# Performance work log

Measured on AMD Instinct MI355X. Metric: run time of the kernel, lower is better.

Reference implementation:

```python
import jax, jax.numpy as jnp
import numpy as np

RADIUS = 0.4
NSHELLS = 3
GSCALE = 0.69314718056 * NSHELLS ** 2  # ln(2)*num_shells^2, as in TFN.__init__
KNN = 32          # patch_size
UNITS = 64        # per-type intertwiner width
STRIDE = 4        # source->target pooling ratio (num_points[i]/num_points[i+1])


def real_sh(d):
    """Real spherical harmonics up to l=3 on unit vectors d[...,3] -> [...,16]."""
    x, y, z = d[..., 0], d[..., 1], d[..., 2]
    x2, y2, z2 = x * x, y * y, z * z
    comps = [
        0.282095 * jnp.ones_like(x),                 # l=0
        0.488603 * y, 0.488603 * z, 0.488603 * x,    # l=1 (y,z,x)
        1.092548 * x * y,                            # l=2
        1.092548 * y * z,
        0.315392 * (3.0 * z2 - 1.0),
        1.092548 * x * z,
        0.546274 * (x2 - y2),
        0.590044 * y * (3.0 * x2 - y2),              # l=3
        2.890611 * x * y * z,
        0.457046 * y * (5.0 * z2 - 1.0),
        0.373176 * z * (5.0 * z2 - 3.0),
        0.457046 * x * (5.0 * z2 - 1.0),
        1.445306 * z * (x2 - y2),
        0.590044 * x * (x2 - 3.0 * y2),
    ]
    return jnp.stack(comps, axis=-1)


def setup_inputs() -> dict:
    key = jax.random.key(0)
    ks = jax.random.split(key, 16)
    B, N, C = 32, 2048, 64
    SC = NSHELLS * C  # channels after shell expansion
    FEAT = 4 * UNITS  # invariant feature dim (types 0..3)
    NUM_CLASSES = 40
    inp = {
        "points": jax.random.normal(ks[0], (B, N, 3), jnp.float32),
        "feats": 0.1 * jax.random.normal(ks[1], (B, N, C), jnp.float32),
        "W0": jax.random.normal(ks[2], (SC, UNITS), jnp.float32) / np.sqrt(SC),
        "b0": jnp.zeros((UNITS,), jnp.float32),
        "W1": jax.random.normal(ks[3], (SC, UNITS), jnp.float32) / np.sqrt(SC),
        "W2": jax.random.normal(ks[4], (SC, UNITS), jnp.float32) / np.sqrt(SC),
        "W3": jax.random.normal(ks[5], (SC, UNITS), jnp.float32) / np.sqrt(SC),
        "Wfc1": jax.random.normal(ks[6], (FEAT, 512), jnp.float32) / np.sqrt(FEAT),
        "bfc1": jnp.zeros((512,), jnp.float32),
        "Wfc2": jax.random.normal(ks[7], (512, 256), jnp.float32) / np.sqrt(512),
        "bfc2": jnp.zeros((256,), jnp.float32),
        "Wsm": jax.random.normal(ks[8], (256, NUM_CLASSES), jnp.float32) / np.sqrt(256),
        "bsm": jnp.zeros((NUM_CLASSES,), jnp.float32),
    }
    return inp


def reference(points, feats, W0, b0, W1, W2, W3, Wfc1, bfc1, Wfc2, bfc2, Wsm, bsm):
    # --- pooling: strided subsample (kd_pooling analogue) ---
    target = points[:, ::STRIDE]                       # [B,M,3]
    # --- ball-query style grouping: knn gather ---
    d2 = jnp.sum((target[:, :, None, :] - points[:, None, :, :]) ** 2, axis=-1)  # [B,M,N]
    _, idx = jax.lax.top_k(-d2, KNN)                   # [B,M,K]
    gat = jax.vmap(lambda a, i: a[i])
    p = gat(points, idx)                               # [B,M,K,3]
    f = gat(feats, idx)                                # [B,M,K,C]
    rel = p - target[:, :, None, :]
    dist = jnp.sqrt(jnp.maximum(jnp.sum(rel * rel, axis=-1), 1e-12))  # [B,M,K]
    dirs = rel / dist[..., None]
    # --- spherical-harmonic Gaussian shell kernels ---
    Y = real_sh(dirs)                                  # [B,M,K,16]
    centers = jnp.linspace(0.0, 1.0, NSHELLS)
    dn = dist / RADIUS
    w = jnp.exp(-GSCALE * (dn[..., None] - centers) ** 2)
    w = w * (dn <= 1.0)[..., None]                     # bounded kernel
    w = w / (jnp.sum(w, axis=2, keepdims=True) + 1e-8)  # normalize over patch
    kern = w[..., :, None] * Y[..., None, :]           # [B,M,K,S,16]
    # --- point conv: contract over patch dim ---
    z = jnp.einsum('bmksp,bmkc->bmpsc', kern, f)       # [B,M,16,S,C]
    B_, M_ = z.shape[:2]
    z = z.reshape(B_, M_, 16, -1)                      # [B,M,16,S*C]
    # --- per-type Dense intertwiners (bias only on type-0) + invariant norms ---
    slabs = [(0, 1, W0, b0), (1, 4, W1, None), (4, 9, W2, None), (9, 16, W3, None)]
    outs = []
    for s, e, W, b in slabs:
        o = z[:, :, s:e, :] @ W
        if b is not None:
            o = o + b
        outs.append(jnp.sqrt(jnp.maximum(jnp.sum(o * o, axis=2), 1e-8)))  # [B,M,U]
    h = jnp.concatenate(outs, axis=-1)                 # [B,M,4U]
    h = jnp.max(h, axis=1)                             # global max pool
    # --- MLP head ---
    h = jax.nn.relu(h @ Wfc1 + bfc1)
    h = jax.nn.relu(h @ Wfc2 + bfc2)
    return jax.nn.softmax(h @ Wsm + bsm, axis=-1)
```

## Files before the change

### kernel.cpp

```cpp
#include <hip/hip_runtime.h>
#include <hip/hip_bf16.h>
#include <math.h>

#define B_ 32
#define N_ 2048
#define C_ 64
#define M_ 512
#define KNN_ 32
#define RADIUS_ 0.4f
#define RCUT2 0.16016f
#define GSCALE_ 6.2383246250f
#define TT 4
#define SEGCAP 40
#define NBLK 4096

typedef __attribute__((ext_vector_type(8))) short bf16x8;
typedef __attribute__((ext_vector_type(4))) float f32x4;
union FragU { uint4 q; bf16x8 h; unsigned int u[4]; };

#define CAND_OFF 0
#define CNT_OFF  1280
#define ZT_ 3144
#define RST 196
#define FSH 560
#define FSL 1616
#define WGT_OFF  12576
#define WGT_TS   96
#define SM_TOTAL 12960

__device__ inline void split2(float a, unsigned& hi, unsigned& lo) {
    unsigned ab = __float_as_uint(a);
    float res = a - __uint_as_float(ab & 0xffff0000u);
    __hip_bfloat16 lb = __float2bfloat16(res);
    hi = ab >> 16;
    lo = *(unsigned short*)&lb;
}

__device__ inline unsigned cvt_pk_bf16(float a, float b) {
    unsigned r;
    asm("v_cvt_pk_bf16_f32 %0, %1, %2" : "=v"(r) : "v"(a), "v"(b));
    return r;
}

__device__ inline void split_pair(float a0, float a1, unsigned& hw, unsigned& lw) {
    hw = cvt_pk_bf16(a0, a1);
    float r0 = a0 - __uint_as_float(hw << 16);
    float r1 = a1 - __uint_as_float(hw & 0xffff0000u);
    lw = cvt_pk_bf16(r0, r1);
}

__device__ inline unsigned pack_hl(float a) {
    unsigned t = cvt_pk_bf16(a, a);
    unsigned hfu = t << 16;
    float res = a - __uint_as_float(hfu);
    return cvt_pk_bf16(__uint_as_float(hfu), res);
}

__global__ __launch_bounds__(256) void wsplit_kernel(
    const float* __restrict__ W0, const float* __restrict__ W1,
    const float* __restrict__ W2, const float* __restrict__ W3,
    uint4* __restrict__ Wb)
{
    int gid = blockIdx.x * 256 + threadIdx.x;
    int lane = gid & 63, frag = gid >> 6;
    int v = frag & 1, nt = (frag >> 1) & 3;
    int ls = frag >> 3, ks = ls % 6, l = ls / 6;
    const float* W = (l==0) ? W0 : (l==1) ? W1 : (l==2) ? W2 : W3;
    int n = nt*16 + (lane & 15), quad = lane >> 4;
    unsigned int d[4];
    #pragma unroll
    for (int dd = 0; dd < 4; ++dd) {
        unsigned int two[2];
        #pragma unroll
        for (int e = 0; e < 2; ++e) {
            int k = ks*32 + quad*8 + dd*2 + e;
            unsigned hi, lo;
            split2(W[k*64 + n], hi, lo);
            two[e] = (v == 0) ? hi : lo;
        }
        d[dd] = two[0] | (two[1] << 16);
    }
    Wb[(size_t)frag*64 + lane] = make_uint4(d[0], d[1], d[2], d[3]);
}

__global__ __launch_bounds__(256, 3) void main_kernel(
    const float* __restrict__ points, const float* __restrict__ feats,
    const float* __restrict__ b0, const uint4* __restrict__ Wb,
    unsigned int* __restrict__ hmax,
    const float* __restrict__ Wfc1, const float* __restrict__ Wfc2,
    float* __restrict__ dummy)
{
    __shared__ __align__(16) float smem[SM_TOTAL];
    __shared__ int sh_nbr[TT][32];
    __shared__ int sh_cnt[TT];
    unsigned int* smemU = (unsigned int*)smem;
    const int tid = threadIdx.x;
    const int b = blockIdx.x >> 7;
    const int mbase = (blockIdx.x & 127) * TT;
    const float* pb = points + (size_t)b * N_ * 3;
    const int wv = tid >> 6, lane = tid & 63;

    float wm1 = Wfc1[(size_t)blockIdx.x*32 + (tid & 31)];
    float wm2 = Wfc2[(size_t)blockIdx.x*32 + (tid & 31)];

    float b0r[4];
    #pragma unroll
    for (int nt = 0; nt < 4; ++nt) b0r[nt] = b0[nt*16 + (lane & 15)];

    {
        unsigned long long* cand = (unsigned long long*)&smem[CAND_OFF];
        int* cntk = (int*)&smem[CNT_OFF];
        float tx[TT], ty[TT], tz[TT];
        #pragma unroll
        for (int c = 0; c < TT; ++c) {
            int m4 = 4*(mbase + c);
            tx[c] = pb[3*m4]; ty[c] = pb[3*m4+1]; tz[c] = pb[3*m4+2];
        }
        float px[8], py[8], pz[8];
        const float* ps = pb + 3*(wv*512 + lane);
        #pragma unroll
        for (int it = 0; it < 8; ++it) {
            px[it] = ps[it*192+0]; py[it] = ps[it*192+1]; pz[it] = ps[it*192+2];
        }
        int bcnt[TT];
        #pragma unroll
        for (int c = 0; c < TT; ++c) bcnt[c] = 0;
        #pragma unroll
        for (int it = 0; it < 8; ++it) {
            int i = wv*512 + it*64 + lane;
            #pragma unroll
            for (int c = 0; c < TT; ++c) {
                float dx = px[it] - tx[c], dy = py[it] - ty[c], dz = pz[it] - tz[c];
                float d2 = fmaf(dx,dx, fmaf(dy,dy, dz*dz));
                bool isc = d2 <= RCUT2;
                unsigned long long mk = __ballot(isc);
                if (isc) {
                    int pos = bcnt[c] + __popcll(mk & ((1ull<<lane)-1ull));
                    if (pos < SEGCAP)
                        cand[(size_t)(wv*TT+c)*SEGCAP + pos] =
                            ((unsigned long long)__float_as_uint(d2) << 32) | (unsigned)i;
                }
                bcnt[c] += __popcll(mk);
            }
        }
        if (lane == 0) {
            #pragma unroll
            for (int c = 0; c < TT; ++c)
                cntk[wv*TT+c] = bcnt[c] < SEGCAP ? bcnt[c] : SEGCAP;
        }
        __syncthreads();
        {
            const int t = wv;
            int c0 = cntk[0*TT+t], c1 = cntk[1*TT+t], c2 = cntk[2*TT+t], c3 = cntk[3*TT+t];
            int o1 = c0, o2 = c0+c1, o3 = c0+c1+c2;
            int C = o3 + c3; C = C < 128 ? C : 128;
            auto fetch = [&](int pos) -> unsigned long long {
                if (pos >= C) return ~0ull;
                int ws = (pos >= o1) + (pos >= o2) + (pos >= o3);
                int base = (ws==0) ? 0 : (ws==1) ? o1 : (ws==2) ? o2 : o3;
                return cand[(size_t)(ws*TT+t)*SEGCAP + (pos - base)];
            };
            unsigned long long kv0 = fetch(lane), kv1 = fetch(64 + lane);
            const unsigned long long lmask = (1ull << lane) - 1ull;
            if (C <= KNN_) {
                if (lane < KNN_) sh_nbr[t][lane] = (lane < C) ? (int)(kv0 & 0xffffffffu) : 0;
                if (lane == 0) sh_cnt[t] = C;
            } else {
                unsigned d0 = (unsigned)(kv0 >> 32);
                unsigned d1 = (unsigned)(kv1 >> 32);
                unsigned thr = 0u;
                for (int bit = 29; bit >= 0; --bit) {
                    unsigned mid = thr | (1u << bit);
                    int cnt = __popcll(__ballot(d0 < mid)) + __popcll(__ballot(d1 < mid));
                    if (cnt < KNN_) thr = mid;
                }
                bool le0 = d0 < thr, le1 = d1 < thr;
                int cntL = __popcll(__ballot(le0)) + __popcll(__ballot(le1));
                int E = KNN_ - cntL;
                unsigned long long me0 = __ballot(d0 == thr);
                unsigned long long me1 = __ballot(d1 == thr);
                int e0 = __popcll(me0);
                bool sel0 = le0 || ((d0 == thr) && (__popcll(me0 & lmask) < E));
                bool sel1 = le1 || ((d1 == thr) && (e0 + __popcll(me1 & lmask) < E));
                unsigned long long ms0 = __ballot(sel0);
                if (sel0) sh_nbr[t][__popcll(ms0 & lmask)] = (int)(kv0 & 0xffffffffu);
                int base0 = __popcll(ms0);
                unsigned long long ms1 = __ballot(sel1);
                if (sel1) sh_nbr[t][base0 + __popcll(ms1 & lmask)] = (int)(kv1 & 0xffffffffu);
                if (lane == 0) sh_cnt[t] = KNN_;
            }
        }
    }
    __syncthreads();

    if (tid < TT*32) {
        int t = tid >> 5, k = tid & 31;
        int n = sh_nbr[t][k];
        int m4 = 4*(mbase + t);
        float x = pb[3*n]   - pb[3*m4];
        float y = pb[3*n+1] - pb[3*m4+1];
        float z = pb[3*n+2] - pb[3*m4+2];
        float d2 = x*x + y*y + z*z;
        float dist = sqrtf(fmaxf(d2, 1e-12f));
        float inv = 1.0f / dist;
        float dx = x*inv, dy = y*inv, dz = z*inv;
        float x2 = dx*dx, y2 = dy*dy, z2 = dz*dz;
        float yv[16];
        yv[0]  = 0.282095f;
        yv[1]  = 0.488603f*dy;  yv[2] = 0.488603f*dz;  yv[3] = 0.488603f*dx;
        yv[4]  = 1.092548f*dx*dy;
        yv[5]  = 1.092548f*dy*dz;
        yv[6]  = 0.315392f*(3.0f*z2-1.0f);
        yv[7]  = 1.092548f*dx*dz;
        yv[8]  = 0.546274f*(x2-y2);
        yv[9]  = 0.590044f*dy*(3.0f*x2-y2);
        yv[10] = 2.890611f*dx*dy*dz;
        yv[11] = 0.457046f*dy*(5.0f*z2-1.0f);
        yv[12] = 0.373176f*dz*(5.0f*z2-3.0f);
        yv[13] = 0.457046f*dx*(5.0f*z2-1.0f);
        yv[14] = 1.445306f*dz*(x2-y2);
        yv[15] = 0.590044f*dx*(x2-3.0f*y2);
        float* Yp = &smem[t*ZT_ + k*17];
        #pragma unroll
        for (int p = 0; p < 16; ++p) Yp[p] = yv[p];
        float dn = dist * (1.0f/RADIUS_);
        bool ok = (k < sh_cnt[t]) && (dn <= 1.0f);
        float w0 = 0.f, w1 = 0.f, w2 = 0.f;
        if (ok) {
            float dd0 = dn, dd1 = dn - 0.5f, dd2 = dn - 1.0f;
            w0 = __expf(-GSCALE_*dd0*dd0);
            w1 = __expf(-GSCALE_*dd1*dd1);
            w2 = __expf(-GSCALE_*dd2*dd2);
        }
        float s0 = w0, s1 = w1, s2 = w2;
        #pragma unroll
        for (int off = 16; off >= 1; off >>= 1) {
            s0 += __shfl_xor(s0, off);
            s1 += __shfl_xor(s1, off);
            s2 += __shfl_xor(s2, off);
        }
        w0 /= (s0 + 1e-8f);
        w1 /= (s1 + 1e-8f);
        w2 /= (s2 + 1e-8f);
        smem[WGT_OFF + t*WGT_TS +      k] = w0;
        smem[WGT_OFF + t*WGT_TS + 32 + k] = w1;
        smem[WGT_OFF + t*WGT_TS + 64 + k] = w2;
    }
    {
        const float* fb = feats + (size_t)b * N_ * C_;
        const int t = wv;
        #pragma unroll
        for (int k2 = 0; k2 < 16; ++k2) {
            float f0 = fb[(size_t)sh_nbr[t][2*k2]   * C_ + lane];
            float f1 = fb[(size_t)sh_nbr[t][2*k2+1] * C_ + lane];
            unsigned hw, lw;
            split_pair(f0, f1, hw, lw);
            smemU[t*ZT_ + FSH + k2*66 + lane] = hw;
            smemU[t*ZT_ + FSL + k2*66 + lane] = lw;
        }
    }
    __syncthreads();

    {
        const int t = wv;
        const int quad = lane >> 4, col = lane & 15;
        float yv8[8];
        #pragma unroll
        for (int d = 0; d < 8; ++d)
            yv8[d] = smem[t*ZT_ + (quad*8 + d)*17 + col];
        FragU ah[3], al[3];
        #pragma unroll
        for (int s = 0; s < 3; ++s) {
            #pragma unroll
            for (int i = 0; i < 4; ++i) {
                float we = smem[WGT_OFF + t*WGT_TS + s*32 + quad*8 + 2*i];
                float wo = smem[WGT_OFF + t*WGT_TS + s*32 + quad*8 + 2*i + 1];
                split_pair(yv8[2*i]*we, yv8[2*i+1]*wo, ah[s].u[i], al[s].u[i]);
            }
        }
        f32x4 acc[3][4];
        #pragma unroll
        for (int s = 0; s < 3; ++s)
            #pragma unroll
            for (int nl = 0; nl < 4; ++nl) acc[s][nl] = (f32x4){0.f,0.f,0.f,0.f};
        #pragma unroll
        for (int nl = 0; nl < 4; ++nl) {
            int n = nl*16 + col;
            FragU bh, bl;
            #pragma unroll
            for (int i = 0; i < 4; ++i) {
                int k2 = quad*4 + i;
                bh.u[i] = smemU[t*ZT_ + FSH + k2*66 + n];
                bl.u[i] = smemU[t*ZT_ + FSL + k2*66 + n];
            }
            #pragma unroll
            for (int s = 0; s < 3; ++s) {
                acc[s][nl] = __builtin_amdgcn_mfma_f32_16x16x32_bf16(ah[s].h, bh.h, acc[s][nl], 0, 0, 0);
                acc[s][nl] = __builtin_amdgcn_mfma_f32_16x16x32_bf16(ah[s].h, bl.h, acc[s][nl], 0, 0, 0);
                acc[s][nl] = __builtin_amdgcn_mfma_f32_16x16x32_bf16(al[s].h, bh.h, acc[s][nl], 0, 0, 0);
            }
        }
        #pragma unroll
        for (int s = 0; s < 3; ++s) {
            #pragma unroll
            for (int nl = 0; nl < 4; ++nl) {
                #pragma unroll
                for (int r = 0; r < 4; ++r) {
                    int p = quad*4 + r;
                    smemU[t*ZT_ + p*RST + s*64 + nl*16 + col] = pack_hl(acc[s][nl][r]);
                }
            }
        }
    }
    __syncthreads();

    {
        const int bp0[4] = {0,1,4,9};
        const int bsz[4] = {1,3,5,7};
        const int band = wv;
        const int sz = bsz[band], p0 = bp0[band];
        const int rows = 2*sz;
        const int quad = lane >> 4, col = lane & 15;
        int gc = col < rows-1 ? col : rows-1;
        int tA = gc >= sz ? 1 : 0;
        int pA = p0 + gc - tA*sz;
        const unsigned baseA = tA*ZT_ + pA*RST;
        const unsigned baseB = baseA + 2*ZT_;
        f32x4 accA[4], accB[4];
        #pragma unroll
        for (int nt = 0; nt < 4; ++nt) {
            accA[nt] = (f32x4){0.f,0.f,0.f,0.f};
            accB[nt] = (f32x4){0.f,0.f,0.f,0.f};
        }

        #pragma unroll
        for (int ks = 0; ks < 6; ++ks) {
            const uint4* zpA = (const uint4*)&smemU[baseA + ks*32 + quad*8];
            const uint4* zpB = (const uint4*)&smemU[baseB + ks*32 + quad*8];
            uint4 a0q = zpA[0], a1q = zpA[1];
            uint4 c0q = zpB[0], c1q = zpB[1];
            FragU ahA, alA, ahB, alB;
            ahA.u[0] = __builtin_amdgcn_perm(a0q.y, a0q.x, 0x05040100u);
            ahA.u[1] = __builtin_amdgcn_perm(a0q.w, a0q.z, 0x05040100u);
            ahA.u[2] = __builtin_amdgcn_perm(a1q.y, a1q.x, 0x05040100u);
            ahA.u[3] = __builtin_amdgcn_perm(a1q.w, a1q.z, 0x05040100u);
            alA.u[0] = __builtin_amdgcn_perm(a0q.y, a0q.x, 0x07060302u);
            alA.u[1] = __builtin_amdgcn_perm(a0q.w, a0q.z, 0x07060302u);
            alA.u[2] = __builtin_amdgcn_perm(a1q.y, a1q.x, 0x07060302u);
            alA.u[3] = __builtin_amdgcn_perm(a1q.w, a1q.z, 0x07060302u);
            ahB.u[0] = __builtin_amdgcn_perm(c0q.y, c0q.x, 0x05040100u);
            ahB.u[1] = __builtin_amdgcn_perm(c0q.w, c0q.z, 0x05040100u);
            ahB.u[2] = __builtin_amdgcn_perm(c1q.y, c1q.x, 0x05040100u);
            ahB.u[3] = __builtin_amdgcn_perm(c1q.w, c1q.z, 0x05040100u);
            alB.u[0] = __builtin_amdgcn_perm(c0q.y, c0q.x, 0x07060302u);
            alB.u[1] = __builtin_amdgcn_perm(c0q.w, c0q.z, 0x07060302u);
            alB.u[2] = __builtin_amdgcn_perm(c1q.y, c1q.x, 0x07060302u);
            alB.u[3] = __builtin_amdgcn_perm(c1q.w, c1q.z, 0x07060302u);
            #pragma unroll
            for (int nt = 0; nt < 4; ++nt) {
                int fbase = ((band*6 + ks)*4 + nt)*2;
                FragU bh, bl;
                bh.q = Wb[(size_t)(fbase + 0)*64 + lane];
                bl.q = Wb[(size_t)(fbase + 1)*64 + lane];
                accA[nt] = __builtin_amdgcn_mfma_f32_16x16x32_bf16(ahA.h, bh.h, accA[nt], 0, 0, 0);
                accA[nt] = __builtin_amdgcn_mfma_f32_16x16x32_bf16(ahA.h, bl.h, accA[nt], 0, 0, 0);
                accA[nt] = __builtin_amdgcn_mfma_f32_16x16x32_bf16(alA.h, bh.h, accA[nt], 0, 0, 0);
                accB[nt] = __builtin_amdgcn_mfma_f32_16x16x32_bf16(ahB.h, bh.h, accB[nt], 0, 0, 0);
                accB[nt] = __builtin_amdgcn_mfma_f32_16x16x32_bf16(ahB.h, bl.h, accB[nt], 0, 0, 0);
                accB[nt] = __builtin_amdgcn_mfma_f32_16x16x32_bf16(alB.h, bh.h, accB[nt], 0, 0, 0);
            }
        }
        float sq[4][4];
        #pragma unroll
        for (int nt = 0; nt < 4; ++nt)
            #pragma unroll
            for (int tg = 0; tg < 4; ++tg) sq[nt][tg] = 0.f;
        #pragma unroll
        for (int r = 0; r < 4; ++r) {
            int row = quad*4 + r;
            bool valid = row < rows;
            int tt = row >= sz ? 1 : 0;
            #pragma unroll
            for (int nt = 0; nt < 4; ++nt) {
                float oA = accA[nt][r], oB = accB[nt][r];
                if (band == 0) { oA += b0r[nt]; oB += b0r[nt]; }
                if (valid) {
                    sq[nt][tt]   += oA*oA;
                    sq[nt][2+tt] += oB*oB;
                }
            }
        }
        #pragma unroll
        for (int nt = 0; nt < 4; ++nt) {
            #pragma unroll
            for (int tg = 0; tg < 4; ++tg) {
                float v = sq[nt][tg];
                v += __shfl_xor(v, 16);
                v += __shfl_xor(v, 32);
                sq[nt][tg] = v;
            }
        }
        if (quad == 0) {
            #pragma unroll
            for (int nt = 0; nt < 4; ++nt) {
                float h0 = sqrtf(fmaxf(sq[nt][0], 1e-8f));
                float h1 = sqrtf(fmaxf(sq[nt][1], 1e-8f));
                float h2 = sqrtf(fmaxf(sq[nt][2], 1e-8f));
                float h3 = sqrtf(fmaxf(sq[nt][3], 1e-8f));
                float mx = fmaxf(fmaxf(h0, h1), fmaxf(h2, h3));
                atomicMax(&hmax[b*256 + band*64 + nt*16 + col],
                          __float_as_uint(mx) ^ 0x80000000u);
            }
        }
    }

    if (__float_as_uint(wm1 + wm2) == 0xdeadbeefu) dummy[0] = wm1;
}

__global__ __launch_bounds__(256) void fc1_kernel(
    const unsigned int* __restrict__ hmaxk,
    const float* __restrict__ Wfc1, const float* __restrict__ bfc1,
    float* __restrict__ t1)
{
    __shared__ float h[256];
    __shared__ float red[4][80];
    const int b = blockIdx.x >> 3, uc = blockIdx.x & 7;
    const int tid = threadIdx.x;
    const int u = tid & 63, iq = tid >> 6;
    h[tid] = __uint_as_float(hmaxk[b*256 + tid] ^ 0x80000000u);
    __syncthreads();
    float acc = 0.f;
    const float* Wp = Wfc1 + uc*64 + u;
    #pragma unroll 8
    for (int i = iq*64; i < iq*64 + 64; ++i)
        acc = fmaf(h[i], Wp[(size_t)i*512], acc);
    red[iq][u] = acc;
    __syncthreads();
    if (iq == 0) {
        float s = red[0][u] + red[1][u] + red[2][u] + red[3][u] + bfc1[uc*64 + u];
        t1[b*512 + uc*64 + u] = fmaxf(s, 0.f);
    }
}

__global__ __launch_bounds__(256) void fc2_kernel(
    const float* __restrict__ t1,
    const float* __restrict__ Wfc2, const float* __restrict__ bfc2,
    float* __restrict__ t2)
{
    __shared__ float t1s[512];
    __shared__ float red[4][80];
    const int b = blockIdx.x >> 2, uc = blockIdx.x & 3;
    const int tid = threadIdx.x;
    const int u = tid & 63, isl = tid >> 6;
    t1s[tid]       = t1[b*512 + tid];
    t1s[256 + tid] = t1[b*512 + 256 + tid];
    __syncthreads();
    float acc = 0.f;
    const float* Wp = Wfc2 + uc*64 + u;
    #pragma unroll 8
    for (int i = isl*128; i < isl*128 + 128; ++i)
        acc = fmaf(t1s[i], Wp[(size_t)i*256], acc);
    red[isl][u] = acc;
    __syncthreads();
    if (isl == 0) {
        float s = red[0][u] + red[1][u] + red[2][u] + red[3][u] + bfc2[uc*64 + u];
        t2[b*256 + uc*64 + u] = fmaxf(s, 0.f);
    }
}

__global__ __launch_bounds__(256) void fc3_kernel(
    const float* __restrict__ t2,
    const float* __restrict__ Wsm, const float* __restrict__ bsm,
    float* __restrict__ out)
{
    __shared__ float t2s[256];
    __shared__ float red[4][80];
    const int b = blockIdx.x;
    const int tid = threadIdx.x;
    const int u = tid & 63, isl = tid >> 6;
    t2s[tid] = t2[b*256 + tid];
    __syncthreads();
    float acc = 0.f;
    if (u < 40) {
        #pragma unroll 8
        for (int i = isl*64; i < isl*64 + 64; ++i)
            acc = fmaf(t2s[i], Wsm[(size_t)i*40 + u], acc);
    }
    red[isl][u] = acc;
    __syncthreads();
    if (tid < 64) {
        float s = red[0][tid] + red[1][tid] + red[2][tid] + red[3][tid];
        float x = (tid < 40) ? (s + bsm[tid]) : -1e30f;
        float mx = x;
        #pragma unroll
        for (int off = 32; off >= 1; off >>= 1) mx = fmaxf(mx, __shfl_xor(mx, off));
        float e = (tid < 40) ? expf(x - mx) : 0.f;
        float ssum = e;
        #pragma unroll
        for (int off = 32; off >= 1; off >>= 1) ssum += __shfl_xor(ssum, off);
        if (tid < 40) out[b*40 + tid] = e / ssum;
    }
}

extern "C" void kernel_launch(void* const* d_in, const int* in_sizes, int n_in,
                              void* d_out, int out_size, void* d_ws, size_t ws_size,
                              hipStream_t stream)
{
    const float* points = (const float*)d_in[0];
    const float* feats  = (const float*)d_in[1];
    const float* W0   = (const float*)d_in[2];
    const float* b0   = (const float*)d_in[3];
    const float* W1   = (const float*)d_in[4];
    const float* W2   = (const float*)d_in[5];
    const float* W3   = (const float*)d_in[6];
    const float* Wfc1 = (const float*)d_in[7];
    const float* bfc1 = (const float*)d_in[8];
    const float* Wfc2 = (const float*)d_in[9];
    const float* bfc2 = (const float*)d_in[10];
    const float* Wsm  = (const float*)d_in[11];
    const float* bsm  = (const float*)d_in[12];
    float* out = (float*)d_out;

    char* ws = (char*)d_ws;
    unsigned int* hmax = (unsigned int*)ws;
    float* t1 = (float*)(ws + 32*1024);
    float* t2 = (float*)(ws + 96*1024);
    float* dummy = (float*)(ws + 120*1024);
    uint4* Wb = (uint4*)(ws + 128*1024);

    wsplit_kernel<<<48, 256, 0, stream>>>(W0, W1, W2, W3, Wb);
    main_kernel<<<NBLK, 256, 0, stream>>>(points, feats, b0, Wb, hmax,
                                          Wfc1, Wfc2, dummy);
    fc1_kernel<<<256, 256, 0, stream>>>(hmax, Wfc1, bfc1, t1);
    fc2_kernel<<<128, 256, 0, stream>>>(t1, Wfc2, bfc2, t2);
    fc3_kernel<<<32, 256, 0, stream>>>(t2, Wsm, bsm, out);
}
```

Measured before the change: 189.4 us.

## Process eight targets per 512-thread block and reuse weight fragments across targets

Doubles targets per block from four to eight, launching half as many blocks of 512 threads. In the MFMA stage each wave handles one band and half the output columns for all eight targets, so each loaded weight fragment feeds four target pairs instead of two. The per-target geometry and spherical-harmonic work is merged into the feature-gather phase, which removes one barrier and lets feature loads overlap with that math. The trade-off is more shared memory per block and lower block-level occupancy (two blocks per CU), plus a longer eight-segment candidate merge.

```diff
diff --git a/kernel.cpp b/kernel.cpp
--- a/kernel.cpp
+++ b/kernel.cpp
@@ -10,23 +10,22 @@
 #define RADIUS_ 0.4f
 #define RCUT2 0.16016f
 #define GSCALE_ 6.2383246250f
-#define TT 4
+#define TT 8
 #define SEGCAP 40
-#define NBLK 4096
+#define NBLK 2048
 
 typedef __attribute__((ext_vector_type(8))) short bf16x8;
 typedef __attribute__((ext_vector_type(4))) float f32x4;
 union FragU { uint4 q; bf16x8 h; unsigned int u[4]; };
 
-#define CAND_OFF 0
-#define CNT_OFF  1280
 #define ZT_ 3144
 #define RST 196
 #define FSH 560
 #define FSL 1616
-#define WGT_OFF  12576
+#define CAND_OFF 18864
+#define WGT_OFF  25152
 #define WGT_TS   96
-#define SM_TOTAL 12960
+#define SM_TOTAL 25920
 
 __device__ inline void split2(float a, unsigned& hi, unsigned& lo) {
     unsigned ab = __float_as_uint(a);
@@ -83,7 +82,7 @@
     Wb[(size_t)frag*64 + lane] = make_uint4(d[0], d[1], d[2], d[3]);
 }
 
-__global__ __launch_bounds__(256, 3) void main_kernel(
+__global__ __launch_bounds__(512, 2) void main_kernel(
     const float* __restrict__ points, const float* __restrict__ feats,
     const float* __restrict__ b0, const uint4* __restrict__ Wb,
     unsigned int* __restrict__ hmax,
@@ -93,41 +92,43 @@
     __shared__ __align__(16) float smem[SM_TOTAL];
     __shared__ int sh_nbr[TT][32];
     __shared__ int sh_cnt[TT];
+    __shared__ int cntk[64];
     unsigned int* smemU = (unsigned int*)smem;
     const int tid = threadIdx.x;
-    const int b = blockIdx.x >> 7;
-    const int mbase = (blockIdx.x & 127) * TT;
+    const int b = blockIdx.x >> 6;
+    const int mbase = (blockIdx.x & 63) * TT;
     const float* pb = points + (size_t)b * N_ * 3;
     const int wv = tid >> 6, lane = tid & 63;
 
-    float wm1 = Wfc1[(size_t)blockIdx.x*32 + (tid & 31)];
-    float wm2 = Wfc2[(size_t)blockIdx.x*32 + (tid & 31)];
-
-    float b0r[4];
+    float wm1 = Wfc1[(size_t)blockIdx.x*64 + (tid & 63)];
+    float wm2 = Wfc2[(size_t)blockIdx.x*64 + (tid & 63)];
+
+    const int nh_pre = wv >> 2;
+    float b0r[2];
     #pragma unroll
-    for (int nt = 0; nt < 4; ++nt) b0r[nt] = b0[nt*16 + (lane & 15)];
+    for (int ntl = 0; ntl < 2; ++ntl)
+        b0r[ntl] = b0[(nh_pre*2 + ntl)*16 + (lane & 15)];
 
     {
         unsigned long long* cand = (unsigned long long*)&smem[CAND_OFF];
-        int* cntk = (int*)&smem[CNT_OFF];
         float tx[TT], ty[TT], tz[TT];
         #pragma unroll
         for (int c = 0; c < TT; ++c) {
             int m4 = 4*(mbase + c);
             tx[c] = pb[3*m4]; ty[c] = pb[3*m4+1]; tz[c] = pb[3*m4+2];
         }
-        float px[8], py[8], pz[8];
-        const float* ps = pb + 3*(wv*512 + lane);
-        #pragma unroll
-        for (int it = 0; it < 8; ++it) {
+        float px[4], py[4], pz[4];
+        const float* ps = pb + 3*(wv*256 + lane);
+        #pragma unroll
+        for (int it = 0; it < 4; ++it) {
             px[it] = ps[it*192+0]; py[it] = ps[it*192+1]; pz[it] = ps[it*192+2];
         }
         int bcnt[TT];
         #pragma unroll
         for (int c = 0; c < TT; ++c) bcnt[c] = 0;
         #pragma unroll
-        for (int it = 0; it < 8; ++it) {
-            int i = wv*512 + it*64 + lane;
+        for (int it = 0; it < 4; ++it) {
+            int i = wv*256 + it*64 + lane;
             #pragma unroll
             for (int c = 0; c < TT; ++c) {
                 float dx = px[it] - tx[c], dy = py[it] - ty[c], dz = pz[it] - tz[c];
@@ -148,121 +149,130 @@
             for (int c = 0; c < TT; ++c)
                 cntk[wv*TT+c] = bcnt[c] < SEGCAP ? bcnt[c] : SEGCAP;
         }
-        __syncthreads();
-        {
-            const int t = wv;
-            int c0 = cntk[0*TT+t], c1 = cntk[1*TT+t], c2 = cntk[2*TT+t], c3 = cntk[3*TT+t];
-            int o1 = c0, o2 = c0+c1, o3 = c0+c1+c2;
-            int C = o3 + c3; C = C < 128 ? C : 128;
-            auto fetch = [&](int pos) -> unsigned long long {
-                if (pos >= C) return ~0ull;
-                int ws = (pos >= o1) + (pos >= o2) + (pos >= o3);
-                int base = (ws==0) ? 0 : (ws==1) ? o1 : (ws==2) ? o2 : o3;
-                return cand[(size_t)(ws*TT+t)*SEGCAP + (pos - base)];
-            };
-            unsigned long long kv0 = fetch(lane), kv1 = fetch(64 + lane);
-            const unsigned long long lmask = (1ull << lane) - 1ull;
-            if (C <= KNN_) {
-                if (lane < KNN_) sh_nbr[t][lane] = (lane < C) ? (int)(kv0 & 0xffffffffu) : 0;
-                if (lane == 0) sh_cnt[t] = C;
-            } else {
-                unsigned d0 = (unsigned)(kv0 >> 32);
-                unsigned d1 = (unsigned)(kv1 >> 32);
-                unsigned thr = 0u;
-                for (int bit = 29; bit >= 0; --bit) {
-                    unsigned mid = thr | (1u << bit);
-                    int cnt = __popcll(__ballot(d0 < mid)) + __popcll(__ballot(d1 < mid));
-                    if (cnt < KNN_) thr = mid;
-                }
-                bool le0 = d0 < thr, le1 = d1 < thr;
-                int cntL = __popcll(__ballot(le0)) + __popcll(__ballot(le1));
-                int E = KNN_ - cntL;
-                unsigned long long me0 = __ballot(d0 == thr);
-                unsigned long long me1 = __ballot(d1 == thr);
-                int e0 = __popcll(me0);
-                bool sel0 = le0 || ((d0 == thr) && (__popcll(me0 & lmask) < E));
-                bool sel1 = le1 || ((d1 == thr) && (e0 + __popcll(me1 & lmask) < E));
-                unsigned long long ms0 = __ballot(sel0);
-                if (sel0) sh_nbr[t][__popcll(ms0 & lmask)] = (int)(kv0 & 0xffffffffu);
-                int base0 = __popcll(ms0);
-                unsigned long long ms1 = __ballot(sel1);
-                if (sel1) sh_nbr[t][base0 + __popcll(ms1 & lmask)] = (int)(kv1 & 0xffffffffu);
-                if (lane == 0) sh_cnt[t] = KNN_;
-            }
-        }
-    }
-    __syncthreads();
-
-    if (tid < TT*32) {
-        int t = tid >> 5, k = tid & 31;
-        int n = sh_nbr[t][k];
-        int m4 = 4*(mbase + t);
-        float x = pb[3*n]   - pb[3*m4];
-        float y = pb[3*n+1] - pb[3*m4+1];
-        float z = pb[3*n+2] - pb[3*m4+2];
-        float d2 = x*x + y*y + z*z;
-        float dist = sqrtf(fmaxf(d2, 1e-12f));
-        float inv = 1.0f / dist;
-        float dx = x*inv, dy = y*inv, dz = z*inv;
-        float x2 = dx*dx, y2 = dy*dy, z2 = dz*dz;
-        float yv[16];
-        yv[0]  = 0.282095f;
-        yv[1]  = 0.488603f*dy;  yv[2] = 0.488603f*dz;  yv[3] = 0.488603f*dx;
-        yv[4]  = 1.092548f*dx*dy;
-        yv[5]  = 1.092548f*dy*dz;
-        yv[6]  = 0.315392f*(3.0f*z2-1.0f);
-        yv[7]  = 1.092548f*dx*dz;
-        yv[8]  = 0.546274f*(x2-y2);
-        yv[9]  = 0.590044f*dy*(3.0f*x2-y2);
-        yv[10] = 2.890611f*dx*dy*dz;
-        yv[11] = 0.457046f*dy*(5.0f*z2-1.0f);
-        yv[12] = 0.373176f*dz*(5.0f*z2-3.0f);
-        yv[13] = 0.457046f*dx*(5.0f*z2-1.0f);
-        yv[14] = 1.445306f*dz*(x2-y2);
-        yv[15] = 0.590044f*dx*(x2-3.0f*y2);
-        float* Yp = &smem[t*ZT_ + k*17];
-        #pragma unroll
-        for (int p = 0; p < 16; ++p) Yp[p] = yv[p];
-        float dn = dist * (1.0f/RADIUS_);
-        bool ok = (k < sh_cnt[t]) && (dn <= 1.0f);
-        float w0 = 0.f, w1 = 0.f, w2 = 0.f;
-        if (ok) {
-            float dd0 = dn, dd1 = dn - 0.5f, dd2 = dn - 1.0f;
-            w0 = __expf(-GSCALE_*dd0*dd0);
-            w1 = __expf(-GSCALE_*dd1*dd1);
-            w2 = __expf(-GSCALE_*dd2*dd2);
-        }
-        float s0 = w0, s1 = w1, s2 = w2;
-        #pragma unroll
-        for (int off = 16; off >= 1; off >>= 1) {
-            s0 += __shfl_xor(s0, off);
-            s1 += __shfl_xor(s1, off);
-            s2 += __shfl_xor(s2, off);
-        }
-        w0 /= (s0 + 1e-8f);
-        w1 /= (s1 + 1e-8f);
-        w2 /= (s2 + 1e-8f);
-        smem[WGT_OFF + t*WGT_TS +      k] = w0;
-        smem[WGT_OFF + t*WGT_TS + 32 + k] = w1;
-        smem[WGT_OFF + t*WGT_TS + 64 + k] = w2;
-    }
+    }
+    __syncthreads();
+
     {
+        unsigned long long* cand = (unsigned long long*)&smem[CAND_OFF];
+        const int t = wv;
+        int c0 = cntk[0*TT+t], c1 = cntk[1*TT+t], c2 = cntk[2*TT+t], c3 = cntk[3*TT+t];
+        int c4 = cntk[4*TT+t], c5 = cntk[5*TT+t], c6 = cntk[6*TT+t], c7 = cntk[7*TT+t];
+        int o1 = c0, o2 = o1+c1, o3 = o2+c2, o4 = o3+c3, o5 = o4+c4, o6 = o5+c5, o7 = o6+c6;
+        int C = o7 + c7; C = C < 128 ? C : 128;
+        auto fetch = [&](int pos) -> unsigned long long {
+            if (pos >= C) return ~0ull;
+            int ws = (pos>=o1)+(pos>=o2)+(pos>=o3)+(pos>=o4)+(pos>=o5)+(pos>=o6)+(pos>=o7);
+            int base = 0;
+            base = pos>=o1 ? o1 : base;
+            base = pos>=o2 ? o2 : base;
+            base = pos>=o3 ? o3 : base;
+            base = pos>=o4 ? o4 : base;
+            base = pos>=o5 ? o5 : base;
+            base = pos>=o6 ? o6 : base;
+            base = pos>=o7 ? o7 : base;
+            return cand[(size_t)(ws*TT+t)*SEGCAP + (pos - base)];
+        };
+        unsigned long long kv0 = fetch(lane), kv1 = fetch(64 + lane);
+        const unsigned long long lmask = (1ull << lane) - 1ull;
+        if (C <= KNN_) {
+            if (lane < KNN_) sh_nbr[t][lane] = (lane < C) ? (int)(kv0 & 0xffffffffu) : 0;
+            if (lane == 0) sh_cnt[t] = C;
+        } else {
+            unsigned d0 = (unsigned)(kv0 >> 32);
+            unsigned d1 = (unsigned)(kv1 >> 32);
+            unsigned thr = 0u;
+            for (int bit = 29; bit >= 0; --bit) {
+                unsigned mid = thr | (1u << bit);
+                int cnt = __popcll(__ballot(d0 < mid)) + __popcll(__ballot(d1 < mid));
+                if (cnt < KNN_) thr = mid;
+            }
+            bool le0 = d0 < thr, le1 = d1 < thr;
+            int cntL = __popcll(__ballot(le0)) + __popcll(__ballot(le1));
+            int E = KNN_ - cntL;
+            unsigned long long me0 = __ballot(d0 == thr);
+            unsigned long long me1 = __ballot(d1 == thr);
+            int e0 = __popcll(me0);
+            bool sel0 = le0 || ((d0 == thr) && (__popcll(me0 & lmask) < E));
+            bool sel1 = le1 || ((d1 == thr) && (e0 + __popcll(me1 & lmask) < E));
+            unsigned long long ms0 = __ballot(sel0);
+            if (sel0) sh_nbr[t][__popcll(ms0 & lmask)] = (int)(kv0 & 0xffffffffu);
+            int base0 = __popcll(ms0);
+            unsigned long long ms1 = __ballot(sel1);
+            if (sel1) sh_nbr[t][base0 + __popcll(ms1 & lmask)] = (int)(kv1 & 0xffffffffu);
+            if (lane == 0) sh_cnt[t] = KNN_;
+        }
+    }
+    __syncthreads();
+
+    {
+        const int t = wv;
         const float* fb = feats + (size_t)b * N_ * C_;
-        const int t = wv;
+        float fv0[16], fv1[16];
         #pragma unroll
         for (int k2 = 0; k2 < 16; ++k2) {
-            float f0 = fb[(size_t)sh_nbr[t][2*k2]   * C_ + lane];
-            float f1 = fb[(size_t)sh_nbr[t][2*k2+1] * C_ + lane];
+            fv0[k2] = fb[(size_t)sh_nbr[t][2*k2]   * C_ + lane];
+            fv1[k2] = fb[(size_t)sh_nbr[t][2*k2+1] * C_ + lane];
+        }
+        if (lane < 32) {
+            int k = lane;
+            int n = sh_nbr[t][k];
+            int m4 = 4*(mbase + t);
+            float x = pb[3*n]   - pb[3*m4];
+            float y = pb[3*n+1] - pb[3*m4+1];
+            float z = pb[3*n+2] - pb[3*m4+2];
+            float d2 = x*x + y*y + z*z;
+            float dist = sqrtf(fmaxf(d2, 1e-12f));
+            float inv = 1.0f / dist;
+            float dx = x*inv, dy = y*inv, dz = z*inv;
+            float x2 = dx*dx, y2 = dy*dy, z2 = dz*dz;
+            float yv[16];
+            yv[0]  = 0.282095f;
+            yv[1]  = 0.488603f*dy;  yv[2] = 0.488603f*dz;  yv[3] = 0.488603f*dx;
+            yv[4]  = 1.092548f*dx*dy;
+            yv[5]  = 1.092548f*dy*dz;
+            yv[6]  = 0.315392f*(3.0f*z2-1.0f);
+            yv[7]  = 1.092548f*dx*dz;
+            yv[8]  = 0.546274f*(x2-y2);
+            yv[9]  = 0.590044f*dy*(3.0f*x2-y2);
+            yv[10] = 2.890611f*dx*dy*dz;
+            yv[11] = 0.457046f*dy*(5.0f*z2-1.0f);
+            yv[12] = 0.373176f*dz*(5.0f*z2-3.0f);
+            yv[13] = 0.457046f*dx*(5.0f*z2-1.0f);
+            yv[14] = 1.445306f*dz*(x2-y2);
+            yv[15] = 0.590044f*dx*(x2-3.0f*y2);
+            float* Yp = &smem[t*ZT_ + k*17];
+            #pragma unroll
+            for (int p = 0; p < 16; ++p) Yp[p] = yv[p];
+            float dn = dist * (1.0f/RADIUS_);
+            bool ok = (k < sh_cnt[t]) && (dn <= 1.0f);
+            float w0 = 0.f, w1 = 0.f, w2 = 0.f;
+            if (ok) {
+                float dd0 = dn, dd1 = dn - 0.5f, dd2 = dn - 1.0f;
+                w0 = __expf(-GSCALE_*dd0*dd0);
+                w1 = __expf(-GSCALE_*dd1*dd1);
+                w2 = __expf(-GSCALE_*dd2*dd2);
+            }
+            float s0 = w0, s1 = w1, s2 = w2;
+            #pragma unroll
+            for (int off = 16; off >= 1; off >>= 1) {
+                s0 += __shfl_xor(s0, off);
+                s1 += __shfl_xor(s1, off);
+                s2 += __shfl_xor(s2, off);
+            }
+            w0 /= (s0 + 1e-8f);
+            w1 /= (s1 + 1e-8f);
+            w2 /= (s2 + 1e-8f);
+            smem[WGT_OFF + t*WGT_TS +      k] = w0;
+            smem[WGT_OFF + t*WGT_TS + 32 + k] = w1;
+            smem[WGT_OFF + t*WGT_TS + 64 + k] = w2;
+        }
+        #pragma unroll
+        for (int k2 = 0; k2 < 16; ++k2) {
             unsigned hw, lw;
-            split_pair(f0, f1, hw, lw);
+            split_pair(fv0[k2], fv1[k2], hw, lw);
             smemU[t*ZT_ + FSH + k2*66 + lane] = hw;
             smemU[t*ZT_ + FSL + k2*66 + lane] = lw;
         }
-    }
-    __syncthreads();
-
-    {
-        const int t = wv;
         const int quad = lane >> 4, col = lane & 15;
         float yv8[8];
         #pragma unroll
@@ -317,99 +327,89 @@
     {
         const int bp0[4] = {0,1,4,9};
         const int bsz[4] = {1,3,5,7};
-        const int band = wv;
+        const int band = wv & 3, nh = wv >> 2;
         const int sz = bsz[band], p0 = bp0[band];
         const int rows = 2*sz;
         const int quad = lane >> 4, col = lane & 15;
         int gc = col < rows-1 ? col : rows-1;
-        int tA = gc >= sz ? 1 : 0;
-        int pA = p0 + gc - tA*sz;
-        const unsigned baseA = tA*ZT_ + pA*RST;
-        const unsigned baseB = baseA + 2*ZT_;
-        f32x4 accA[4], accB[4];
-        #pragma unroll
-        for (int nt = 0; nt < 4; ++nt) {
-            accA[nt] = (f32x4){0.f,0.f,0.f,0.f};
-            accB[nt] = (f32x4){0.f,0.f,0.f,0.f};
-        }
+        int tl = gc >= sz ? 1 : 0;
+        int pA = p0 + gc - tl*sz;
+        const unsigned base0 = tl*ZT_ + pA*RST;
+        f32x4 acc[4][2];
+        #pragma unroll
+        for (int ti = 0; ti < 4; ++ti)
+            #pragma unroll
+            for (int ntl = 0; ntl < 2; ++ntl) acc[ti][ntl] = (f32x4){0.f,0.f,0.f,0.f};
 
         #pragma unroll
         for (int ks = 0; ks < 6; ++ks) {
-            const uint4* zpA = (const uint4*)&smemU[baseA + ks*32 + quad*8];
-            const uint4* zpB = (const uint4*)&smemU[baseB + ks*32 + quad*8];
-            uint4 a0q = zpA[0], a1q = zpA[1];
-            uint4 c0q = zpB[0], c1q = zpB[1];
-            FragU ahA, alA, ahB, alB;
-            ahA.u[0] = __builtin_amdgcn_perm(a0q.y, a0q.x, 0x05040100u);
-            ahA.u[1] = __builtin_amdgcn_perm(a0q.w, a0q.z, 0x05040100u);
-            ahA.u[2] = __builtin_amdgcn_perm(a1q.y, a1q.x, 0x05040100u);
-            ahA.u[3] = __builtin_amdgcn_perm(a1q.w, a1q.z, 0x05040100u);
-            alA.u[0] = __builtin_amdgcn_perm(a0q.y, a0q.x, 0x07060302u);
-            alA.u[1] = __builtin_amdgcn_perm(a0q.w, a0q.z, 0x07060302u);
-            alA.u[2] = __builtin_amdgcn_perm(a1q.y, a1q.x, 0x07060302u);
-            alA.u[3] = __builtin_amdgcn_perm(a1q.w, a1q.z, 0x07060302u);
-            ahB.u[0] = __builtin_amdgcn_perm(c0q.y, c0q.x, 0x05040100u);
-            ahB.u[1] = __builtin_amdgcn_perm(c0q.w, c0q.z, 0x05040100u);
-            ahB.u[2] = __builtin_amdgcn_perm(c1q.y, c1q.x, 0x05040100u);
-            ahB.u[3] = __builtin_amdgcn_perm(c1q.w, c1q.z, 0x05040100u);
-            alB.u[0] = __builtin_amdgcn_perm(c0q.y, c0q.x, 0x07060302u);
-            alB.u[1] = __builtin_amdgcn_perm(c0q.w, c0q.z, 0x07060302u);
-            alB.u[2] = __builtin_amdgcn_perm(c1q.y, c1q.x, 0x07060302u);
-            alB.u[3] = __builtin_amdgcn_perm(c1q.w, c1q.z, 0x07060302u);
-            #pragma unroll
-            for (int nt = 0; nt < 4; ++nt) {
-                int fbase = ((band*6 + ks)*4 + nt)*2;
+            FragU ah[4], al[4];
+            #pragma unroll
+            for (int ti = 0; ti < 4; ++ti) {
+                const uint4* zp = (const uint4*)&smemU[base0 + ti*2*ZT_ + ks*32 + quad*8];
+                uint4 q0 = zp[0], q1 = zp[1];
+                ah[ti].u[0] = __builtin_amdgcn_perm(q0.y, q0.x, 0x05040100u);
+                ah[ti].u[1] = __builtin_amdgcn_perm(q0.w, q0.z, 0x05040100u);
+                ah[ti].u[2] = __builtin_amdgcn_perm(q1.y, q1.x, 0x05040100u);
+                ah[ti].u[3] = __builtin_amdgcn_perm(q1.w, q1.z, 0x05040100u);
+                al[ti].u[0] = __builtin_amdgcn_perm(q0.y, q0.x, 0x07060302u);
+                al[ti].u[1] = __builtin_amdgcn_perm(q0.w, q0.z, 0x07060302u);
+                al[ti].u[2] = __builtin_amdgcn_perm(q1.y, q1.x, 0x07060302u);
+                al[ti].u[3] = __builtin_amdgcn_perm(q1.w, q1.z, 0x07060302u);
+            }
+            #pragma unroll
+            for (int ntl = 0; ntl < 2; ++ntl) {
+                int fbase = ((band*6 + ks)*4 + nh*2 + ntl)*2;
                 FragU bh, bl;
                 bh.q = Wb[(size_t)(fbase + 0)*64 + lane];
                 bl.q = Wb[(size_t)(fbase + 1)*64 + lane];
-                accA[nt] = __builtin_amdgcn_mfma_f32_16x16x32_bf16(ahA.h, bh.h, accA[nt], 0, 0, 0);
-                accA[nt] = __builtin_amdgcn_mfma_f32_16x16x32_bf16(ahA.h, bl.h, accA[nt], 0, 0, 0);
-                accA[nt] = __builtin_amdgcn_mfma_f32_16x16x32_bf16(alA.h, bh.h, accA[nt], 0, 0, 0);
-                accB[nt] = __builtin_amdgcn_mfma_f32_16x16x32_bf16(ahB.h, bh.h, accB[nt], 0, 0, 0);
-                accB[nt] = __builtin_amdgcn_mfma_f32_16x16x32_bf16(ahB.h, bl.h, accB[nt], 0, 0, 0);
-                accB[nt] = __builtin_amdgcn_mfma_f32_16x16x32_bf16(alB.h, bh.h, accB[nt], 0, 0, 0);
-            }
-        }
-        float sq[4][4];
-        #pragma unroll
-        for (int nt = 0; nt < 4; ++nt)
-            #pragma unroll
-            for (int tg = 0; tg < 4; ++tg) sq[nt][tg] = 0.f;
+                #pragma unroll
+                for (int ti = 0; ti < 4; ++ti) {
+                    acc[ti][ntl] = __builtin_amdgcn_mfma_f32_16x16x32_bf16(ah[ti].h, bh.h, acc[ti][ntl], 0, 0, 0);
+                    acc[ti][ntl] = __builtin_amdgcn_mfma_f32_16x16x32_bf16(ah[ti].h, bl.h, acc[ti][ntl], 0, 0, 0);
+                    acc[ti][ntl] = __builtin_amdgcn_mfma_f32_16x16x32_bf16(al[ti].h, bh.h, acc[ti][ntl], 0, 0, 0);
+                }
+            }
+        }
+        float sq[2][8];
+        #pragma unroll
+        for (int ntl = 0; ntl < 2; ++ntl)
+            #pragma unroll
+            for (int tg = 0; tg < 8; ++tg) sq[ntl][tg] = 0.f;
         #pragma unroll
         for (int r = 0; r < 4; ++r) {
             int row = quad*4 + r;
             bool valid = row < rows;
-            int tt = row >= sz ? 1 : 0;
-            #pragma unroll
-            for (int nt = 0; nt < 4; ++nt) {
-                float oA = accA[nt][r], oB = accB[nt][r];
-                if (band == 0) { oA += b0r[nt]; oB += b0r[nt]; }
-                if (valid) {
-                    sq[nt][tt]   += oA*oA;
-                    sq[nt][2+tt] += oB*oB;
+            int tl2 = row >= sz ? 1 : 0;
+            #pragma unroll
+            for (int ti = 0; ti < 4; ++ti) {
+                #pragma unroll
+                for (int ntl = 0; ntl < 2; ++ntl) {
+                    float o = acc[ti][ntl][r];
+                    if (band == 0) o += b0r[ntl];
+                    if (valid) sq[ntl][ti*2 + tl2] += o*o;
                 }
             }
         }
         #pragma unroll
-        for (int nt = 0; nt < 4; ++nt) {
-            #pragma unroll
-            for (int tg = 0; tg < 4; ++tg) {
-                float v = sq[nt][tg];
+        for (int ntl = 0; ntl < 2; ++ntl) {
+            #pragma unroll
+            for (int tg = 0; tg < 8; ++tg) {
+                float v = sq[ntl][tg];
                 v += __shfl_xor(v, 16);
                 v += __shfl_xor(v, 32);
-                sq[nt][tg] = v;
+                sq[ntl][tg] = v;
             }
         }
         if (quad == 0) {
             #pragma unroll
-            for (int nt = 0; nt < 4; ++nt) {
-                float h0 = sqrtf(fmaxf(sq[nt][0], 1e-8f));
-                float h1 = sqrtf(fmaxf(sq[nt][1], 1e-8f));
-                float h2 = sqrtf(fmaxf(sq[nt][2], 1e-8f));
-                float h3 = sqrtf(fmaxf(sq[nt][3], 1e-8f));
-                float mx = fmaxf(fmaxf(h0, h1), fmaxf(h2, h3));
-                atomicMax(&hmax[b*256 + band*64 + nt*16 + col],
-                          __float_as_uint(mx) ^ 0x80000000u);
+            for (int ntl = 0; ntl < 2; ++ntl) {
+                float m = sq[ntl][0];
+                #pragma unroll
+                for (int tg = 1; tg < 8; ++tg) m = fmaxf(m, sq[ntl][tg]);
+                float h = sqrtf(fmaxf(m, 1e-8f));
+                atomicMax(&hmax[b*256 + band*64 + (nh*2 + ntl)*16 + col],
+                          __float_as_uint(h) ^ 0x80000000u);
             }
         }
     }
@@ -529,7 +529,7 @@
     uint4* Wb = (uint4*)(ws + 128*1024);
 
     wsplit_kernel<<<48, 256, 0, stream>>>(W0, W1, W2, W3, Wb);
-    main_kernel<<<NBLK, 256, 0, stream>>>(points, feats, b0, Wb, hmax,
+    main_kernel<<<NBLK, 512, 0, stream>>>(points, feats, b0, Wb, hmax,
                                           Wfc1, Wfc2, dummy);
     fc1_kernel<<<256, 256, 0, stream>>>(hmax, Wfc1, bfc1, t1);
     fc2_kernel<<<128, 256, 0, stream>>>(t1, Wfc2, bfc2, t2);
```

Result: slower. 203.0 us (+7.2%).
